# Kernel optimization log

Hardware: AMD Instinct MI355X
Metric: run time of the kernel (lower is better)

## Reference

```python
import jax, jax.numpy as jnp
import numpy as np

# dims: B batch, T frames, N tokens/frame, C embed, H heads, D=C//H, MEM memory slots
B, T, N, C = 8, 16, 196, 768
H = 8
D = C // H
MEM = 196          # mem_size; with N=196 -> _init_t = 1, M stays == MEM
HID = 4 * C        # mlp_ratio * embed_dim
STD = 0.02


def _mlp(x, w1, b1, w2, b2):
    # timm-style Mlp: fc1 -> GELU -> fc2 (dropout = 0)
    return jax.nn.gelu(x @ w1 + b1, approximate=False) @ w2 + b2


def _ln(x, w, b, eps=1e-5):
    mu = jnp.mean(x, axis=-1, keepdims=True)
    var = jnp.var(x, axis=-1, keepdims=True)
    return (x - mu) * jax.lax.rsqrt(var + eps) * w + b


def setup_inputs() -> dict:
    key = jax.random.key(0)
    ks = jax.random.split(key, 10)
    f32 = jnp.float32
    return {
        "cur_fea": jax.random.normal(ks[0], (B, T, N, C), f32),
        "norm1_w": jnp.ones((C,), f32), "norm1_b": jnp.zeros((C,), f32),
        "norm2_w": jnp.ones((C,), f32), "norm2_b": jnp.zeros((C,), f32),
        # c_func: Mlp(2C -> 4C -> C)
        "c_w1": jax.random.normal(ks[1], (2 * C, HID), f32) * STD, "c_b1": jnp.zeros((HID,), f32),
        "c_w2": jax.random.normal(ks[2], (HID, C), f32) * STD, "c_b2": jnp.zeros((C,), f32),
        # m_func: Mlp(C -> 4C -> C)
        "m_w1": jax.random.normal(ks[3], (C, HID), f32) * STD, "m_b1": jnp.zeros((HID,), f32),
        "m_w2": jax.random.normal(ks[4], (HID, C), f32) * STD, "m_b2": jnp.zeros((C,), f32),
        # post_func: Mlp(C -> 4C -> C)
        "p_w1": jax.random.normal(ks[5], (C, HID), f32) * STD, "p_b1": jnp.zeros((HID,), f32),
        "p_w2": jax.random.normal(ks[6], (HID, C), f32) * STD, "p_b2": jnp.zeros((C,), f32),
        # ProjectDotDistance: per-head q(c_global) . k(mem) * scale -> sigmoid
        "q_w": jax.random.normal(ks[7], (C, C), f32) * STD, "q_b": jnp.zeros((C,), f32),
        "k_w": jax.random.normal(ks[8], (C, C), f32) * STD, "k_b": jnp.zeros((C,), f32),
    }


def reference(cur_fea, norm1_w, norm1_b, norm2_w, norm2_b,
              c_w1, c_b1, c_w2, c_b2, m_w1, m_b1, m_w2, m_b2,
              p_w1, p_b1, p_w2, p_b2, q_w, q_b, k_w, k_b):
    x = _ln(cur_fea, norm1_w, norm1_b)                       # [B,T,N,C]
    # T*N > mem_size, _init_t = MEM // N = 1 -> init memory = frame 0 (no grad, torch.no_grad)
    init_mem = jax.lax.stop_gradient(x[:, 0].reshape(B, MEM, C))
    scale = D ** -0.5

    def step(mem, fea):                                      # mem [B,MEM,C], fea [B,N,C]
        ap = jnp.mean(mem, axis=1, keepdims=True)            # [B,1,C]
        cg = _mlp(jnp.concatenate([fea, jnp.broadcast_to(ap, fea.shape)], axis=-1),
                  c_w1, c_b1, c_w2, c_b2)                    # [B,N,C]
        memh = _mlp(mem, m_w1, m_b1, m_w2, m_b2).reshape(B, MEM, H, D).transpose(0, 2, 1, 3)  # [B,H,M,D]
        q = (cg @ q_w + q_b).reshape(B, N, H, D).transpose(0, 2, 1, 3)    # [B,H,N,D]
        k = (mem @ k_w + k_b).reshape(B, MEM, H, D).transpose(0, 2, 1, 3) # [B,H,M,D]
        o = jax.nn.sigmoid(jnp.einsum('bhnd,bhmd->bhnm', q, k) * scale)   # [B,H,N,M]
        cgh = cg.reshape(B, N, H, D).transpose(0, 2, 1, 3)               # [B,H,N,D]
        c = jnp.einsum('bhnm,bhnd->bmhd', o, cgh).reshape(B, MEM, C)
        c = _mlp(c, p_w1, p_b1, p_w2, p_b2)
        # mean_N((1-o) * broadcast(memh)) == mean_N(1-o) * memh (memh indep of N)
        gate = jnp.mean(1.0 - o, axis=2)                     # [B,H,M]
        og = (gate[..., None] * memh).transpose(0, 2, 1, 3).reshape(B, MEM, C)
        new_mem = _ln(c + og, norm2_w, norm2_b)
        return new_mem, None

    fea_seq = x[:, 1:].transpose(1, 0, 2, 3)                 # [T-1,B,N,C]
    final_mem, _ = jax.lax.scan(step, init_mem, fea_seq)
    return final_mem                                         # [B,MEM,C]
```

## Files before the change

### kernel.cpp

```cpp
#include <hip/hip_runtime.h>
#include <hip/hip_bf16.h>
#include <math.h>

constexpr int B_   = 8;
constexpr int T_   = 16;
constexpr int N_   = 196;
constexpr int C_   = 768;
constexpr int H_   = 8;
constexpr int D_   = 96;
constexpr int M_   = 196;
constexpr int HID_ = 3072;
constexpr int ROWS_ = B_ * N_;
constexpr int MP_   = 1664;

typedef __hip_bfloat16 bf16;
typedef __attribute__((ext_vector_type(8))) short bf16x8;
typedef __attribute__((ext_vector_type(4))) float f32x4;

__device__ __forceinline__ float b2f(bf16 x) { return __bfloat162float(x); }
__device__ __forceinline__ short bf2s(bf16 x) { union { bf16 b; short s; } u; u.b = x; return u.s; }
__device__ __forceinline__ float s2f(short x) { union { bf16 b; short s; } u; u.s = x; return __bfloat162float(u.b); }

#define GL2LDS(g, l) __builtin_amdgcn_global_load_lds( \
    (__attribute__((address_space(1))) void*)(g), \
    (__attribute__((address_space(3))) void*)(l), 16, 0, 0)

__device__ __forceinline__ void hard_barrier() {
    asm volatile("" ::: "memory");
    __builtin_amdgcn_s_barrier();
    asm volatile("" ::: "memory");
}

__device__ __forceinline__ float block_reduce_sum256(float v, float* sdata) {
    int tid = threadIdx.x;
    sdata[tid] = v;
    __syncthreads();
    for (int s = 128; s > 0; s >>= 1) {
        if (tid < s) sdata[tid] += sdata[tid + s];
        __syncthreads();
    }
    float r = sdata[0];
    __syncthreads();
    return r;
}

struct TEnt { const float* W; bf16* Wt; int K; int N; int tiles; };
struct TEnts { TEnt e[8]; };

__global__ __launch_bounds__(256) void transpose_all_kernel(TEnts tds)
{
    __shared__ float tile[32][33];
    int local = blockIdx.x;
    int i = 0;
    while (i < 7 && local >= tds.e[i].tiles) { local -= tds.e[i].tiles; ++i; }
    TEnt g = tds.e[i];
    int ntx = g.N / 32;
    int n0 = (local % ntx) * 32, k0 = (local / ntx) * 32;
    int tx = threadIdx.x & 31, ty = threadIdx.x >> 5;
#pragma unroll
    for (int r = 0; r < 32; r += 8)
        tile[ty + r][tx] = g.W[(size_t)(k0 + ty + r) * g.N + n0 + tx];
    __syncthreads();
#pragma unroll
    for (int r = 0; r < 32; r += 8)
        g.Wt[(size_t)(n0 + ty + r) * g.K + k0 + tx] = __float2bfloat16(tile[tx][ty + r]);
}

__global__ __launch_bounds__(256) void cvt_kernel(const float* __restrict__ W,
                                                  bf16* __restrict__ o, int n)
{
    int i = blockIdx.x * 256 + threadIdx.x;
    if (i < n) o[i] = __float2bfloat16(W[i]);
}

__global__ __launch_bounds__(256) void ln_frame_kernel(
    const float* __restrict__ cur, int t,
    const float* __restrict__ w, const float* __restrict__ bia,
    bf16* __restrict__ mem_bf)
{
    __shared__ float sdata[256];
    int row = blockIdx.x;
    int b = row / N_, n = row % N_;
    const float* src = cur + (((size_t)b * T_ + t) * N_ + n) * C_;
    float x[3];
    float sum = 0.f, sumsq = 0.f;
#pragma unroll
    for (int i = 0; i < 3; i++) {
        int c = threadIdx.x + i * 256;
        x[i] = src[c];
        sum += x[i]; sumsq += x[i] * x[i];
    }
    sum = block_reduce_sum256(sum, sdata);
    sumsq = block_reduce_sum256(sumsq, sdata);
    float mu = sum * (1.0f / C_);
    float var = sumsq * (1.0f / C_) - mu * mu;
    float rs = rsqrtf(var + 1e-5f);
#pragma unroll
    for (int i = 0; i < 3; i++) {
        int c = threadIdx.x + i * 256;
        mem_bf[(size_t)row * C_ + c] = __float2bfloat16((x[i] - mu) * rs * w[c] + bia[c]);
    }
}

__global__ __launch_bounds__(768) void ap_kernel(const bf16* __restrict__ mem,
                                                 float* __restrict__ ap)
{
    int b = blockIdx.x;
    int c = threadIdx.x;
    const bf16* p = mem + (size_t)b * M_ * C_ + c;
    float s = 0.f;
    for (int m = 0; m < M_; m++) s += b2f(p[(size_t)m * C_]);
    ap[b * C_ + c] = s * (1.0f / M_);
}

__global__ __launch_bounds__(256) void build_cat_kernel(
    const float* __restrict__ cur, int t,
    const float* __restrict__ w, const float* __restrict__ bia,
    const float* __restrict__ ap, bf16* __restrict__ cat)
{
    __shared__ float sdata[256];
    int row = blockIdx.x;
    int b = row / N_, n = row % N_;
    const float* src = cur + (((size_t)b * T_ + t) * N_ + n) * C_;
    float x[3];
    float sum = 0.f, sumsq = 0.f;
#pragma unroll
    for (int i = 0; i < 3; i++) {
        int c = threadIdx.x + i * 256;
        x[i] = src[c];
        sum += x[i]; sumsq += x[i] * x[i];
    }
    sum = block_reduce_sum256(sum, sdata);
    sumsq = block_reduce_sum256(sumsq, sdata);
    float mu = sum * (1.0f / C_);
    float var = sumsq * (1.0f / C_) - mu * mu;
    float rs = rsqrtf(var + 1e-5f);
    bf16* dstrow = cat + (size_t)row * (2 * C_);
#pragma unroll
    for (int i = 0; i < 3; i++) {
        int c = threadIdx.x + i * 256;
        dstrow[c] = __float2bfloat16((x[i] - mu) * rs * w[c] + bia[c]);
        dstrow[C_ + c] = __float2bfloat16(ap[b * C_ + c]);
    }
}

struct GemmDesc {
    const bf16* A; const bf16* W; const float* bias; bf16* out;
    int K; int N; int ymax; int gelu;
};
struct GemmDescs { GemmDesc d[4]; };

template <int BN>
__global__ __launch_bounds__(256) void mfma_gemm_multi(GemmDescs ds)
{
    constexpr int BM = 128;
    constexpr int TI = 4;
    constexpr int TJ = (BN / 2) / 16;
    constexpr int ABYTES = BM * 128;
    constexpr int BBYTES = BN * 128;
    constexpr int AR = ABYTES / 4096;
    constexpr int BR = BBYTES / 4096;
    constexpr int NL = AR + BR;
    __shared__ short As[2 * BM * 64];
    __shared__ short Bs[2 * BN * 64];

    GemmDesc g = ds.d[blockIdx.z];
    if ((int)blockIdx.y >= g.ymax) return;

    int tid = threadIdx.x;
    int wid = tid >> 6;
    int lane = tid & 63;
    int quad = lane >> 4, l15 = lane & 15;
    int row0 = blockIdx.x * BM;
    int col0 = blockIdx.y * BN;
    int wm = (wid >> 1) * 64;
    int wn = (wid & 1) * (BN / 2);

    f32x4 acc[TI][TJ] = {};

    const char* Ab = (const char*)g.A;
    const char* Wb = (const char*)g.W;
    const size_t Kb = (size_t)g.K * 2;
    const int base = wid * 1024;

    auto stage = [&](int k0, int sel) {
        char* Ad = (char*)As + sel * ABYTES;
        char* Bd = (char*)Bs + sel * BBYTES;
#pragma unroll
        for (int r = 0; r < AR; r++) {
            int o = r * 4096 + base + lane * 16;
            int row = o >> 7, cs = (o >> 4) & 7;
            int kc = cs ^ (row & 7);
            GL2LDS(Ab + (size_t)(row0 + row) * Kb + (size_t)k0 * 2 + kc * 16, Ad + o);
        }
#pragma unroll
        for (int r = 0; r < BR; r++) {
            int o = r * 4096 + base + lane * 16;
            int row = o >> 7, cs = (o >> 4) & 7;
            int kc = cs ^ (row & 7);
            GL2LDS(Wb + (size_t)(col0 + row) * Kb + (size_t)k0 * 2 + kc * 16, Bd + o);
        }
    };

    const int nk = g.K / 64;
    stage(0, 0);
    for (int ki = 0; ki < nk; ki++) {
        int sel = ki & 1;
        if (ki + 1 < nk) {
            stage((ki + 1) * 64, sel ^ 1);
            asm volatile("s_waitcnt vmcnt(%0)" :: "n"(NL) : "memory");
        } else {
            asm volatile("s_waitcnt vmcnt(0)" ::: "memory");
        }
        hard_barrier();
        const bf16x8* Av = (const bf16x8*)(As + sel * BM * 64);
        const bf16x8* Bv = (const bf16x8*)(Bs + sel * BN * 64);
        bf16x8 af[TI][2], bfr[TJ][2];
#pragma unroll
        for (int i = 0; i < TI; i++) {
            int r = wm + i * 16 + l15;
#pragma unroll
            for (int hh = 0; hh < 2; hh++)
                af[i][hh] = Av[r * 8 + ((hh * 4 + quad) ^ (r & 7))];
        }
#pragma unroll
        for (int j = 0; j < TJ; j++) {
            int r = wn + j * 16 + l15;
#pragma unroll
            for (int hh = 0; hh < 2; hh++)
                bfr[j][hh] = Bv[r * 8 + ((hh * 4 + quad) ^ (r & 7))];
        }
#pragma unroll
        for (int hh = 0; hh < 2; hh++)
#pragma unroll
            for (int i = 0; i < TI; i++)
#pragma unroll
                for (int j = 0; j < TJ; j++)
                    acc[i][j] = __builtin_amdgcn_mfma_f32_16x16x32_bf16(
                        af[i][hh], bfr[j][hh], acc[i][j], 0, 0, 0);
        hard_barrier();
    }

#pragma unroll
    for (int i = 0; i < TI; i++) {
        int gr = row0 + wm + i * 16 + quad * 4;
#pragma unroll
        for (int j = 0; j < TJ; j++) {
            int gc = col0 + wn + j * 16 + l15;
            float bv = g.bias ? g.bias[gc] : 0.0f;
#pragma unroll
            for (int r = 0; r < 4; r++) {
                float v = acc[i][j][r] + bv;
                if (g.gelu) v = 0.5f * v * (1.0f + erff(v * 0.7071067811865475f));
                g.out[(size_t)(gr + r) * g.N + gc] = __float2bfloat16(v);
            }
        }
    }
}

__global__ __launch_bounds__(256) void mfma_gemm_splitk(
    const bf16* __restrict__ A, const bf16* __restrict__ Wt,
    float* __restrict__ part, int K)
{
    constexpr int BM = 128;
    constexpr int BN = 64;
    constexpr int TI = 4;
    constexpr int TJ = 2;
    constexpr int ABYTES = BM * 128, BBYTES = BN * 128;
    constexpr int AR = 4, BR = 2, NL = 6;
    __shared__ short As[2 * BM * 64];
    __shared__ short Bs[2 * BN * 64];

    int tid = threadIdx.x;
    int wid = tid >> 6;
    int lane = tid & 63;
    int quad = lane >> 4, l15 = lane & 15;
    int row0 = blockIdx.x * BM;
    int col0 = blockIdx.y * BN;
    int wm = (wid >> 1) * 64;
    int wn = (wid & 1) * 32;
    int kh = K >> 1;
    int kbeg = blockIdx.z * kh;

    f32x4 acc[TI][TJ] = {};
    const char* Ab = (const char*)A;
    const char* Wb = (const char*)Wt;
    const size_t Kb = (size_t)K * 2;
    const int base = wid * 1024;

    auto stage = [&](int k0, int sel) {
        char* Ad = (char*)As + sel * ABYTES;
        char* Bd = (char*)Bs + sel * BBYTES;
#pragma unroll
        for (int r = 0; r < AR; r++) {
            int o = r * 4096 + base + lane * 16;
            int row = o >> 7, cs = (o >> 4) & 7;
            int kc = cs ^ (row & 7);
            GL2LDS(Ab + (size_t)(row0 + row) * Kb + (size_t)k0 * 2 + kc * 16, Ad + o);
        }
#pragma unroll
        for (int r = 0; r < BR; r++) {
            int o = r * 4096 + base + lane * 16;
            int row = o >> 7, cs = (o >> 4) & 7;
            int kc = cs ^ (row & 7);
            GL2LDS(Wb + (size_t)(col0 + row) * Kb + (size_t)k0 * 2 + kc * 16, Bd + o);
        }
    };

    const int nk = kh / 64;
    stage(kbeg, 0);
    for (int ki = 0; ki < nk; ki++) {
        int sel = ki & 1;
        if (ki + 1 < nk) {
            stage(kbeg + (ki + 1) * 64, sel ^ 1);
            asm volatile("s_waitcnt vmcnt(%0)" :: "n"(NL) : "memory");
        } else {
            asm volatile("s_waitcnt vmcnt(0)" ::: "memory");
        }
        hard_barrier();
        const bf16x8* Av = (const bf16x8*)(As + sel * BM * 64);
        const bf16x8* Bv = (const bf16x8*)(Bs + sel * BN * 64);
        bf16x8 af[TI][2], bfr[TJ][2];
#pragma unroll
        for (int i = 0; i < TI; i++) {
            int r = wm + i * 16 + l15;
#pragma unroll
            for (int hh = 0; hh < 2; hh++)
                af[i][hh] = Av[r * 8 + ((hh * 4 + quad) ^ (r & 7))];
        }
#pragma unroll
        for (int j = 0; j < TJ; j++) {
            int r = wn + j * 16 + l15;
#pragma unroll
            for (int hh = 0; hh < 2; hh++)
                bfr[j][hh] = Bv[r * 8 + ((hh * 4 + quad) ^ (r & 7))];
        }
#pragma unroll
        for (int hh = 0; hh < 2; hh++)
#pragma unroll
            for (int i = 0; i < TI; i++)
#pragma unroll
                for (int j = 0; j < TJ; j++)
                    acc[i][j] = __builtin_amdgcn_mfma_f32_16x16x32_bf16(
                        af[i][hh], bfr[j][hh], acc[i][j], 0, 0, 0);
        hard_barrier();
    }

    float* outp = part + (size_t)blockIdx.z * MP_ * C_;
#pragma unroll
    for (int i = 0; i < TI; i++) {
        int gr = row0 + wm + i * 16 + quad * 4;
#pragma unroll
        for (int j = 0; j < TJ; j++) {
            int gc = col0 + wn + j * 16 + l15;
#pragma unroll
            for (int r = 0; r < 4; r++)
                outp[(size_t)(gr + r) * C_ + gc] = acc[i][j][r];
        }
    }
}

__global__ __launch_bounds__(256) void b2q_kernel(
    const float* __restrict__ c_b2, const float* __restrict__ q_b,
    const bf16* __restrict__ W2q_t, float* __restrict__ b2q)
{
    __shared__ float sdata[256];
    int n = blockIdx.x;
    const bf16* row = W2q_t + (size_t)n * HID_;
    float s = 0.f;
    for (int j = threadIdx.x; j < HID_; j += 256) s += c_b2[j] * b2f(row[j]);
    s = block_reduce_sum256(s, sdata);
    if (threadIdx.x == 0) b2q[n] = s + q_b[n];
}

__global__ __launch_bounds__(512) void attn_mfma_kernel(
    const bf16* __restrict__ q, const bf16* __restrict__ k,
    const bf16* __restrict__ cg, bf16* __restrict__ cbuf,
    float* __restrict__ gate)
{
    constexpr int KS = 104;
    constexpr int PSS = 40;
    __shared__ short Ks[64 * KS];
    __shared__ short Qs[32 * KS];
    __shared__ short CGt[96 * PSS];
    __shared__ short Ph[64 * PSS];
    __shared__ short Pl[64 * PSS];
    __shared__ float gred[8][64];

    const int mt = blockIdx.x, h = blockIdx.y, b = blockIdx.z;
    const int m0 = (mt < 3) ? mt * 64 : (M_ - 64);
    const int tid = threadIdx.x;
    const int w = tid >> 6, lane = tid & 63;
    const int quad = lane >> 4, l15 = lane & 15;
    const int wm = w >> 1;
    const int wh = w & 1;
    const float scale = 0.10206207261596575f;

    const bf16* qp = q  + (size_t)b * N_ * C_ + h * D_;
    const bf16* kp = k  + (size_t)b * M_ * C_ + h * D_;
    const bf16* cp = cg + (size_t)b * N_ * C_ + h * D_;

    for (int idx = tid; idx < 64 * 12; idx += 512) {
        int r = idx / 12, c = idx % 12;
        *(bf16x8*)(Ks + r * KS + c * 8) =
            *(const bf16x8*)(kp + (size_t)(m0 + r) * C_ + c * 8);
    }

    f32x4 acc[3] = {};
    float gacc = 0.f;

    const bf16x8 ZEROV = {0, 0, 0, 0, 0, 0, 0, 0};
    bf16x8 qv = ZEROV, cgv = ZEROV;
    const bool active = tid < 32 * 12;
    const int qrow = tid / 12, qcol = (tid % 12) * 8;
    const int cgn = tid & 31, cgd = (tid >> 5) * 8;

    auto issue = [&](int n0) {
        if (!active) return;
        int nq = n0 + qrow;
        qv = (nq < N_) ? *(const bf16x8*)(qp + (size_t)nq * C_ + qcol) : ZEROV;
        int nc = n0 + cgn;
        cgv = (nc < N_) ? *(const bf16x8*)(cp + (size_t)nc * C_ + cgd) : ZEROV;
    };
    auto stage = [&]() {
        if (!active) return;
        *(bf16x8*)(Qs + qrow * KS + qcol) = qv;
#pragma unroll
        for (int i = 0; i < 8; i++) CGt[(cgd + i) * PSS + cgn] = cgv[i];
    };

    issue(0);
    for (int nt = 0; nt < 7; nt++) {
        stage();
        __syncthreads();
        if (nt < 6) issue((nt + 1) * 32);

        f32x4 s4 = {};
#pragma unroll
        for (int kk = 0; kk < 3; kk++) {
            bf16x8 af = *(const bf16x8*)(Ks + (wm * 16 + l15) * KS + kk * 32 + quad * 8);
            bf16x8 bq = *(const bf16x8*)(Qs + (wh * 16 + l15) * KS + kk * 32 + quad * 8);
            s4 = __builtin_amdgcn_mfma_f32_16x16x32_bf16(af, bq, s4, 0, 0, 0);
        }
        const int nglob = nt * 32 + wh * 16 + l15;
#pragma unroll
        for (int r = 0; r < 4; r++) {
            float p = (nglob < N_) ? 1.f / (1.f + expf(-s4[r] * scale)) : 0.f;
            bf16 hb = __float2bfloat16(p);
            bf16 lb = __float2bfloat16(p - __bfloat162float(hb));
            int po = (wm * 16 + quad * 4 + r) * PSS + wh * 16 + l15;
            Ph[po] = bf2s(hb);
            Pl[po] = bf2s(lb);
        }
        __syncthreads();

        {
            const short* ph = Ph + lane * PSS + w * 4;
            const short* pl = Pl + lane * PSS + w * 4;
#pragma unroll
            for (int u = 0; u < 4; u++) gacc += s2f(ph[u]) + s2f(pl[u]);
        }
        bf16x8 pa = *(const bf16x8*)(Ph + (wm * 16 + l15) * PSS + quad * 8);
        bf16x8 pb = *(const bf16x8*)(Pl + (wm * 16 + l15) * PSS + quad * 8);
#pragma unroll
        for (int dt = 0; dt < 3; dt++) {
            bf16x8 bcg = *(const bf16x8*)(CGt + (wh * 48 + dt * 16 + l15) * PSS + quad * 8);
            acc[dt] = __builtin_amdgcn_mfma_f32_16x16x32_bf16(pa, bcg, acc[dt], 0, 0, 0);
            acc[dt] = __builtin_amdgcn_mfma_f32_16x16x32_bf16(pb, bcg, acc[dt], 0, 0, 0);
        }
        __syncthreads();
    }

#pragma unroll
    for (int dt = 0; dt < 3; dt++)
#pragma unroll
        for (int r = 0; r < 4; r++) {
            int m = m0 + wm * 16 + quad * 4 + r;
            cbuf[((size_t)b * M_ + m) * C_ + h * D_ + wh * 48 + dt * 16 + l15] =
                __float2bfloat16(acc[dt][r]);
        }
    gred[w][lane] = gacc;
    __syncthreads();
    if (tid < 64) {
        float g = 0.f;
#pragma unroll
        for (int s = 0; s < 8; s++) g += gred[s][tid];
        gate[((size_t)b * H_ + h) * M_ + m0 + tid] = 1.f - g * (1.0f / N_);
    }
}

__global__ __launch_bounds__(256) void final_kernel(
    const float* __restrict__ part, const float* __restrict__ p_b2,
    const float* __restrict__ gate, const bf16* __restrict__ memh,
    const float* __restrict__ w, const float* __restrict__ bia,
    bf16* __restrict__ mem_bf, float* __restrict__ outp)
{
    __shared__ float sdata[256];
    int row = blockIdx.x;
    int b = row / M_, m = row % M_;
    float x[3];
    float sum = 0.f, sumsq = 0.f;
#pragma unroll
    for (int i = 0; i < 3; i++) {
        int c = threadIdx.x + i * 256;
        int h = c / D_;
        float v = part[(size_t)row * C_ + c] + part[(size_t)MP_ * C_ + (size_t)row * C_ + c]
                + p_b2[c]
                + gate[(b * H_ + h) * M_ + m] * b2f(memh[(size_t)row * C_ + c]);
        x[i] = v;
        sum += v; sumsq += v * v;
    }
    sum = block_reduce_sum256(sum, sdata);
    sumsq = block_reduce_sum256(sumsq, sdata);
    float mu = sum * (1.0f / C_);
    float var = sumsq * (1.0f / C_) - mu * mu;
    float rs = rsqrtf(var + 1e-5f);
#pragma unroll
    for (int i = 0; i < 3; i++) {
        int c = threadIdx.x + i * 256;
        float v = (x[i] - mu) * rs * w[c] + bia[c];
        mem_bf[(size_t)row * C_ + c] = __float2bfloat16(v);
        if (outp) outp[(size_t)row * C_ + c] = v;
    }
}

extern "C" void kernel_launch(void* const* d_in, const int* in_sizes, int n_in,
                              void* d_out, int out_size, void* d_ws, size_t ws_size,
                              hipStream_t stream)
{
    const float* cur_fea = (const float*)d_in[0];
    const float* n1w = (const float*)d_in[1];
    const float* n1b = (const float*)d_in[2];
    const float* n2w = (const float*)d_in[3];
    const float* n2b = (const float*)d_in[4];
    const float* c_w1 = (const float*)d_in[5];
    const float* c_b1 = (const float*)d_in[6];
    const float* c_w2 = (const float*)d_in[7];
    const float* c_b2 = (const float*)d_in[8];
    const float* m_w1 = (const float*)d_in[9];
    const float* m_b1 = (const float*)d_in[10];
    const float* m_w2 = (const float*)d_in[11];
    const float* m_b2 = (const float*)d_in[12];
    const float* p_w1 = (const float*)d_in[13];
    const float* p_b1 = (const float*)d_in[14];
    const float* p_w2 = (const float*)d_in[15];
    const float* p_b2 = (const float*)d_in[16];
    const float* q_w = (const float*)d_in[17];
    const float* q_b = (const float*)d_in[18];
    const float* k_w = (const float*)d_in[19];
    const float* k_b = (const float*)d_in[20];

    size_t off = 0;
    char* base = (char*)d_ws;
    auto carve = [&](size_t bytes) -> char* {
        char* r = base + off;
        off += (bytes + 255) & ~(size_t)255;
        return r;
    };
    bf16* cw1t = (bf16*)carve((size_t)HID_ * (2 * C_) * 2);
    bf16* cw2t = (bf16*)carve((size_t)C_ * HID_ * 2);
    bf16* mw1t = (bf16*)carve((size_t)HID_ * C_ * 2);
    bf16* mw2t = (bf16*)carve((size_t)C_ * HID_ * 2);
    bf16* pw1t = (bf16*)carve((size_t)HID_ * C_ * 2);
    bf16* pw2t = (bf16*)carve((size_t)C_ * HID_ * 2);
    bf16* qwt  = (bf16*)carve((size_t)C_ * C_ * 2);
    bf16* kwt  = (bf16*)carve((size_t)C_ * C_ * 2);
    bf16* mem_bf = (bf16*)carve((size_t)MP_ * C_ * 2);
    char* catreg = carve((size_t)MP_ * 2 * C_ * 2);
    bf16* cat = (bf16*)catreg;
    bf16* qb  = (bf16*)catreg;
    bf16* kb  = (bf16*)catreg + (size_t)MP_ * C_;
    bf16* hid_c = (bf16*)carve((size_t)MP_ * HID_ * 2);
    char* hidm_reg = carve((size_t)MP_ * HID_ * 2);
    bf16*  hid_m = (bf16*)hidm_reg;
    float* part  = (float*)hidm_reg;
    bf16* cg    = (bf16*)carve((size_t)MP_ * C_ * 2);
    bf16* cbuf  = (bf16*)carve((size_t)MP_ * C_ * 2);
    bf16* memh  = (bf16*)carve((size_t)MP_ * C_ * 2);
    float* ap   = (float*)carve((size_t)B_ * C_ * 4);
    float* gateb = (float*)carve((size_t)B_ * H_ * M_ * 4);
    float* b2qb  = (float*)carve((size_t)C_ * 4);
    bf16* W2q_t = (bf16*)carve((size_t)C_ * HID_ * 2);
    const bool fuse_q = (off <= ws_size);

    const dim3 blk(256);

    {
        TEnts tds;
        tds.e[0] = { c_w1, cw1t, 2 * C_, HID_, (HID_ / 32) * ((2 * C_) / 32) };
        tds.e[1] = { c_w2, cw2t, HID_, C_, (C_ / 32) * (HID_ / 32) };
        tds.e[2] = { m_w1, mw1t, C_, HID_, (HID_ / 32) * (C_ / 32) };
        tds.e[3] = { m_w2, mw2t, HID_, C_, (C_ / 32) * (HID_ / 32) };
        tds.e[4] = { p_w1, pw1t, C_, HID_, (HID_ / 32) * (C_ / 32) };
        tds.e[5] = { p_w2, pw2t, HID_, C_, (C_ / 32) * (HID_ / 32) };
        tds.e[6] = { q_w, qwt, C_, C_, (C_ / 32) * (C_ / 32) };
        tds.e[7] = { k_w, kwt, C_, C_, (C_ / 32) * (C_ / 32) };
        int total = 4608 + 2304 * 5 + 576 * 2;
        transpose_all_kernel<<<total, blk, 0, stream>>>(tds);
    }

    if (fuse_q) {
        bf16* cw2nt = hid_c;
        cvt_kernel<<<(HID_ * C_ + 255) / 256, blk, 0, stream>>>(c_w2, cw2nt, HID_ * C_);
        GemmDescs ds;
        ds.d[0] = { qwt, cw2nt, nullptr, W2q_t, C_, HID_, HID_ / 128, 0 };
        ds.d[1] = ds.d[0]; ds.d[2] = ds.d[0]; ds.d[3] = ds.d[0];
        mfma_gemm_multi<128><<<dim3(C_ / 128, HID_ / 128, 1), blk, 0, stream>>>(ds);
        b2q_kernel<<<C_, blk, 0, stream>>>(c_b2, q_b, W2q_t, b2qb);
    }

    ln_frame_kernel<<<ROWS_, blk, 0, stream>>>(cur_fea, 0, n1w, n1b, mem_bf);

    for (int t = 1; t < T_; t++) {
        ap_kernel<<<B_, 768, 0, stream>>>(mem_bf, ap);
        build_cat_kernel<<<ROWS_, blk, 0, stream>>>(cur_fea, t, n1w, n1b, ap, cat);

        {
            GemmDescs ds;
            ds.d[0] = { cat,    cw1t, c_b1, hid_c, 2 * C_, HID_, HID_ / 128, 1 };
            ds.d[1] = { mem_bf, mw1t, m_b1, hid_m, C_,     HID_, HID_ / 128, 1 };
            ds.d[2] = ds.d[0]; ds.d[3] = ds.d[0];
            mfma_gemm_multi<128><<<dim3(MP_ / 128, HID_ / 128, 2), blk, 0, stream>>>(ds);
        }
        {
            GemmDescs ds;
            ds.d[0] = { hid_c,  cw2t, c_b2, cg,   HID_, C_, C_ / 64, 0 };
            ds.d[1] = { hid_m,  mw2t, m_b2, memh, HID_, C_, C_ / 64, 0 };
            ds.d[2] = { mem_bf, kwt,  k_b,  kb,   C_,   C_, C_ / 64, 0 };
            ds.d[3] = { hid_c,  W2q_t, b2qb, qb,  HID_, C_, C_ / 64, 0 };
            mfma_gemm_multi<64><<<dim3(MP_ / 128, C_ / 64, fuse_q ? 4 : 3), blk, 0, stream>>>(ds);
        }
        if (!fuse_q) {
            GemmDescs ds;
            ds.d[0] = { cg, qwt, q_b, qb, C_, C_, C_ / 64, 0 };
            ds.d[1] = ds.d[0]; ds.d[2] = ds.d[0]; ds.d[3] = ds.d[0];
            mfma_gemm_multi<64><<<dim3(MP_ / 128, C_ / 64, 1), blk, 0, stream>>>(ds);
        }
        attn_mfma_kernel<<<dim3(4, H_, B_), dim3(512), 0, stream>>>(qb, kb, cg, cbuf, gateb);
        {
            GemmDescs ds;
            ds.d[0] = { cbuf, pw1t, p_b1, hid_c, C_, HID_, HID_ / 64, 1 };
            ds.d[1] = ds.d[0]; ds.d[2] = ds.d[0]; ds.d[3] = ds.d[0];
            mfma_gemm_multi<64><<<dim3(MP_ / 128, HID_ / 64, 1), blk, 0, stream>>>(ds);
        }
        mfma_gemm_splitk<<<dim3(MP_ / 128, C_ / 64, 2), blk, 0, stream>>>(hid_c, pw2t, part, HID_);
        final_kernel<<<ROWS_, blk, 0, stream>>>(part, p_b2, gateb, memh, n2w, n2b,
                                                mem_bf, (t == T_ - 1) ? (float*)d_out : nullptr);
    }
}
```

Measured before the change: 2.936 ms.

## Fuse memory average pooling via atomics and move K projection into first GEMM

```diff
diff --git a/kernel.cpp b/kernel.cpp
--- a/kernel.cpp
+++ b/kernel.cpp
@@ -31,6 +31,7 @@
     asm volatile("" ::: "memory");
 }
 
+
 __device__ __forceinline__ float block_reduce_sum256(float v, float* sdata) {
     int tid = threadIdx.x;
     sdata[tid] = v;
@@ -76,7 +77,7 @@
 __global__ __launch_bounds__(256) void ln_frame_kernel(
     const float* __restrict__ cur, int t,
     const float* __restrict__ w, const float* __restrict__ bia,
-    bf16* __restrict__ mem_bf)
+    bf16* __restrict__ mem_bf, float* __restrict__ app)
 {
     __shared__ float sdata[256];
     int row = blockIdx.x;
@@ -98,25 +99,16 @@
 #pragma unroll
     for (int i = 0; i < 3; i++) {
         int c = threadIdx.x + i * 256;
-        mem_bf[(size_t)row * C_ + c] = __float2bfloat16((x[i] - mu) * rs * w[c] + bia[c]);
-    }
-}
-
-__global__ __launch_bounds__(768) void ap_kernel(const bf16* __restrict__ mem,
-                                                 float* __restrict__ ap)
-{
-    int b = blockIdx.x;
-    int c = threadIdx.x;
-    const bf16* p = mem + (size_t)b * M_ * C_ + c;
-    float s = 0.f;
-    for (int m = 0; m < M_; m++) s += b2f(p[(size_t)m * C_]);
-    ap[b * C_ + c] = s * (1.0f / M_);
+        bf16 hv = __float2bfloat16((x[i] - mu) * rs * w[c] + bia[c]);
+        mem_bf[(size_t)row * C_ + c] = hv;
+        atomicAdd(&app[(size_t)b * C_ + c], b2f(hv));
+    }
 }
 
 __global__ __launch_bounds__(256) void build_cat_kernel(
     const float* __restrict__ cur, int t,
     const float* __restrict__ w, const float* __restrict__ bia,
-    const float* __restrict__ ap, bf16* __restrict__ cat)
+    const float* __restrict__ app, bf16* __restrict__ cat)
 {
     __shared__ float sdata[256];
     int row = blockIdx.x;
@@ -140,7 +132,7 @@
     for (int i = 0; i < 3; i++) {
         int c = threadIdx.x + i * 256;
         dstrow[c] = __float2bfloat16((x[i] - mu) * rs * w[c] + bia[c]);
-        dstrow[C_ + c] = __float2bfloat16(ap[b * C_ + c]);
+        dstrow[C_ + c] = __float2bfloat16(app[(size_t)b * C_ + c] * (1.0f / M_));
     }
 }
 
@@ -493,7 +485,7 @@
     const float* __restrict__ part, const float* __restrict__ p_b2,
     const float* __restrict__ gate, const bf16* __restrict__ memh,
     const float* __restrict__ w, const float* __restrict__ bia,
-    bf16* __restrict__ mem_bf, float* __restrict__ outp)
+    bf16* __restrict__ mem_bf, float* __restrict__ app, float* __restrict__ outp)
 {
     __shared__ float sdata[256];
     int row = blockIdx.x;
@@ -519,7 +511,9 @@
     for (int i = 0; i < 3; i++) {
         int c = threadIdx.x + i * 256;
         float v = (x[i] - mu) * rs * w[c] + bia[c];
-        mem_bf[(size_t)row * C_ + c] = __float2bfloat16(v);
+        bf16 hv = __float2bfloat16(v);
+        mem_bf[(size_t)row * C_ + c] = hv;
+        atomicAdd(&app[(size_t)b * C_ + c], b2f(hv));
         if (outp) outp[(size_t)row * C_ + c] = v;
     }
 }
@@ -577,11 +571,13 @@
     bf16* cg    = (bf16*)carve((size_t)MP_ * C_ * 2);
     bf16* cbuf  = (bf16*)carve((size_t)MP_ * C_ * 2);
     bf16* memh  = (bf16*)carve((size_t)MP_ * C_ * 2);
-    float* ap   = (float*)carve((size_t)B_ * C_ * 4);
+    float* app  = (float*)carve((size_t)B_ * C_ * 4);
     float* gateb = (float*)carve((size_t)B_ * H_ * M_ * 4);
     float* b2qb  = (float*)carve((size_t)C_ * 4);
     bf16* W2q_t = (bf16*)carve((size_t)C_ * HID_ * 2);
     const bool fuse_q = (off <= ws_size);
+    bf16* kb2  = (bf16*)carve((size_t)MP_ * C_ * 2);
+    const bool fuse_k = (off <= ws_size);
 
     const dim3 blk(256);
 
@@ -609,26 +605,31 @@
         b2q_kernel<<<C_, blk, 0, stream>>>(c_b2, q_b, W2q_t, b2qb);
     }
 
-    ln_frame_kernel<<<ROWS_, blk, 0, stream>>>(cur_fea, 0, n1w, n1b, mem_bf);
+    hipMemsetAsync(app, 0, (size_t)B_ * C_ * 4, stream);
+    ln_frame_kernel<<<ROWS_, blk, 0, stream>>>(cur_fea, 0, n1w, n1b, mem_bf, app);
 
     for (int t = 1; t < T_; t++) {
-        ap_kernel<<<B_, 768, 0, stream>>>(mem_bf, ap);
-        build_cat_kernel<<<ROWS_, blk, 0, stream>>>(cur_fea, t, n1w, n1b, ap, cat);
+        build_cat_kernel<<<ROWS_, blk, 0, stream>>>(cur_fea, t, n1w, n1b, app, cat);
+        hipMemsetAsync(app, 0, (size_t)B_ * C_ * 4, stream);
 
         {
             GemmDescs ds;
             ds.d[0] = { cat,    cw1t, c_b1, hid_c, 2 * C_, HID_, HID_ / 128, 1 };
             ds.d[1] = { mem_bf, mw1t, m_b1, hid_m, C_,     HID_, HID_ / 128, 1 };
-            ds.d[2] = ds.d[0]; ds.d[3] = ds.d[0];
-            mfma_gemm_multi<128><<<dim3(MP_ / 128, HID_ / 128, 2), blk, 0, stream>>>(ds);
+            ds.d[2] = { mem_bf, kwt,  k_b,  kb2,   C_,     C_,   C_ / 128,   0 };
+            ds.d[3] = ds.d[0];
+            mfma_gemm_multi<128><<<dim3(MP_ / 128, HID_ / 128, fuse_k ? 3 : 2),
+                                   blk, 0, stream>>>(ds);
         }
         {
             GemmDescs ds;
-            ds.d[0] = { hid_c,  cw2t, c_b2, cg,   HID_, C_, C_ / 64, 0 };
-            ds.d[1] = { hid_m,  mw2t, m_b2, memh, HID_, C_, C_ / 64, 0 };
-            ds.d[2] = { mem_bf, kwt,  k_b,  kb,   C_,   C_, C_ / 64, 0 };
-            ds.d[3] = { hid_c,  W2q_t, b2qb, qb,  HID_, C_, C_ / 64, 0 };
-            mfma_gemm_multi<64><<<dim3(MP_ / 128, C_ / 64, fuse_q ? 4 : 3), blk, 0, stream>>>(ds);
+            int z = 0;
+            ds.d[z++] = { hid_c,  cw2t, c_b2, cg,   HID_, C_, C_ / 64, 0 };
+            ds.d[z++] = { hid_m,  mw2t, m_b2, memh, HID_, C_, C_ / 64, 0 };
+            if (!fuse_k) ds.d[z++] = { mem_bf, kwt, k_b, kb, C_, C_, C_ / 64, 0 };
+            if (fuse_q)  ds.d[z++] = { hid_c, W2q_t, b2qb, qb, HID_, C_, C_ / 64, 0 };
+            for (int f = z; f < 4; f++) ds.d[f] = ds.d[0];
+            mfma_gemm_multi<64><<<dim3(MP_ / 128, C_ / 64, z), blk, 0, stream>>>(ds);
         }
         if (!fuse_q) {
             GemmDescs ds;
@@ -636,7 +637,8 @@
             ds.d[1] = ds.d[0]; ds.d[2] = ds.d[0]; ds.d[3] = ds.d[0];
             mfma_gemm_multi<64><<<dim3(MP_ / 128, C_ / 64, 1), blk, 0, stream>>>(ds);
         }
-        attn_mfma_kernel<<<dim3(4, H_, B_), dim3(512), 0, stream>>>(qb, kb, cg, cbuf, gateb);
+        attn_mfma_kernel<<<dim3(4, H_, B_), dim3(512), 0, stream>>>(
+            qb, fuse_k ? kb2 : kb, cg, cbuf, gateb);
         {
             GemmDescs ds;
             ds.d[0] = { cbuf, pw1t, p_b1, hid_c, C_, HID_, HID_ / 64, 1 };
@@ -645,6 +647,7 @@
         }
         mfma_gemm_splitk<<<dim3(MP_ / 128, C_ / 64, 2), blk, 0, stream>>>(hid_c, pw2t, part, HID_);
         final_kernel<<<ROWS_, blk, 0, stream>>>(part, p_b2, gateb, memh, n2w, n2b,
-                                                mem_bf, (t == T_ - 1) ? (float*)d_out : nullptr);
-    }
-}
+                                                mem_bf, app,
+                                                (t == T_ - 1) ? (float*)d_out : nullptr);
+    }
+}
```

Measured after the change: 2.793 ms. 4.9% less time.
